# Kernel tuning notes

Hardware: AMD Instinct MI355X
Metric: run time of the kernel (lower is better)

Reference implementation:

```python
import jax, jax.numpy as jnp
import numpy as np

D = 512; H = 8; L = 6; DFF = 2048; V = 32000
B = 2; S_SRC = 1024; S_TRG = 1024
PAD_ID = 0
DH = D // H

def posenc(S, d):
    pos = np.arange(S)[:, None].astype(np.float32)
    i = np.arange(0, d, 2)[None, :].astype(np.float32)
    ang = pos / (10000.0 ** (i / d))
    pe = np.zeros((S, d), np.float32)
    pe[:, 0::2] = np.sin(ang)
    pe[:, 1::2] = np.cos(ang)
    return jnp.asarray(pe)

def layernorm(x, s, b):
    m = jnp.mean(x, -1, keepdims=True)
    v = jnp.var(x, -1, keepdims=True)
    return (x - m) * jax.lax.rsqrt(v + 1e-5) * s + b

def split_heads(x):
    b, s, _ = x.shape
    return x.reshape(b, s, H, DH).transpose(0, 2, 1, 3)  # [B,H,S,DH]

def merge_heads(x):
    b, h, s, dh = x.shape
    return x.transpose(0, 2, 1, 3).reshape(b, s, h * dh)

def attn(q, k, v, mask):
    # q,k,v: [B,H,Sq,DH]/[B,H,Sk,DH]; mask True = blocked, broadcastable to [B,H,Sq,Sk]
    scores = jnp.einsum('bhqd,bhkd->bhqk', q, k) * (DH ** -0.5)
    scores = jnp.where(mask, -1e9, scores)
    p = jax.nn.softmax(scores, axis=-1)
    return merge_heads(jnp.einsum('bhqk,bhkd->bhqd', p, v))

def setup_inputs() -> dict:
    key = jax.random.key(0)
    ks = iter(jax.random.split(key, 64))
    g = lambda shape, s=0.02: (jax.random.normal(next(ks), shape, jnp.float32) * s)
    inp = {}
    inp['batch_src'] = jax.random.randint(next(ks), (B, S_SRC), 0, V, jnp.int32)
    inp['trg_teacher'] = jax.random.randint(next(ks), (B, S_TRG), 0, V, jnp.int32)
    inp['src_emb'] = g((V, D)); inp['trg_emb'] = g((V, D))
    inp['fc_w'] = g((D, V)); inp['fc_b'] = jnp.zeros((V,), jnp.float32)
    # encoder layer stacks [L, ...]
    inp['enc_wqkv'] = g((L, D, 3 * D)); inp['enc_wo'] = g((L, D, D))
    inp['enc_ln1s'] = jnp.ones((L, D)); inp['enc_ln1b'] = jnp.zeros((L, D))
    inp['enc_w1'] = g((L, D, DFF)); inp['enc_b1'] = jnp.zeros((L, DFF))
    inp['enc_w2'] = g((L, DFF, D)); inp['enc_b2'] = jnp.zeros((L, D))
    inp['enc_ln2s'] = jnp.ones((L, D)); inp['enc_ln2b'] = jnp.zeros((L, D))
    # decoder layer stacks
    inp['dec_wqkv'] = g((L, D, 3 * D)); inp['dec_wo'] = g((L, D, D))
    inp['dec_ln1s'] = jnp.ones((L, D)); inp['dec_ln1b'] = jnp.zeros((L, D))
    inp['dec_wq'] = g((L, D, D)); inp['dec_wkv'] = g((L, D, 2 * D))
    inp['dec_woc'] = g((L, D, D))
    inp['dec_ln2s'] = jnp.ones((L, D)); inp['dec_ln2b'] = jnp.zeros((L, D))
    inp['dec_w1'] = g((L, D, DFF)); inp['dec_b1'] = jnp.zeros((L, DFF))
    inp['dec_w2'] = g((L, DFF, D)); inp['dec_b2'] = jnp.zeros((L, D))
    inp['dec_ln3s'] = jnp.ones((L, D)); inp['dec_ln3b'] = jnp.zeros((L, D))
    return inp

def reference(batch_src, trg_teacher, src_emb, trg_emb, fc_w, fc_b,
              enc_wqkv, enc_wo, enc_ln1s, enc_ln1b, enc_w1, enc_b1, enc_w2, enc_b2, enc_ln2s, enc_ln2b,
              dec_wqkv, dec_wo, dec_ln1s, dec_ln1b, dec_wq, dec_wkv, dec_woc, dec_ln2s, dec_ln2b,
              dec_w1, dec_b1, dec_w2, dec_b2, dec_ln3s, dec_ln3b):
    enc_mask = (batch_src == PAD_ID)[:, None, None, :]             # [B,1,1,S_src]
    causal = jnp.triu(jnp.ones((S_TRG, S_TRG), bool), 1)[None, None]  # [1,1,S,S]

    # ---- encoder ----
    x = src_emb[batch_src] * (D ** 0.5) + posenc(S_SRC, D)

    def enc_layer(x, p):
        wqkv, wo, l1s, l1b, w1, b1, w2, b2, l2s, l2b = p
        q, k, v = jnp.split(x @ wqkv, 3, axis=-1)
        o = attn(split_heads(q), split_heads(k), split_heads(v), enc_mask) @ wo
        x = layernorm(x + o, l1s, l1b)
        h = jax.nn.relu(x @ w1 + b1) @ w2 + b2
        return layernorm(x + h, l2s, l2b), None

    enc_out, _ = jax.lax.scan(enc_layer, x,
        (enc_wqkv, enc_wo, enc_ln1s, enc_ln1b, enc_w1, enc_b1, enc_w2, enc_b2, enc_ln2s, enc_ln2b))

    # ---- decoder (teacher forcing) ----
    y = trg_emb[trg_teacher] * (D ** 0.5) + posenc(S_TRG, D)

    def dec_layer(y, p):
        (wqkv, wo, l1s, l1b, wq, wkv, woc, l2s, l2b, w1, b1, w2, b2, l3s, l3b) = p
        q, k, v = jnp.split(y @ wqkv, 3, axis=-1)
        o = attn(split_heads(q), split_heads(k), split_heads(v), causal) @ wo
        y = layernorm(y + o, l1s, l1b)
        qc = y @ wq
        kc, vc = jnp.split(enc_out @ wkv, 2, axis=-1)
        oc = attn(split_heads(qc), split_heads(kc), split_heads(vc), enc_mask) @ woc
        y = layernorm(y + oc, l2s, l2b)
        h = jax.nn.relu(y @ w1 + b1) @ w2 + b2
        return layernorm(y + h, l3s, l3b), None

    dec_out, _ = jax.lax.scan(dec_layer, y,
        (dec_wqkv, dec_wo, dec_ln1s, dec_ln1b, dec_wq, dec_wkv, dec_woc, dec_ln2s, dec_ln2b,
         dec_w1, dec_b1, dec_w2, dec_b2, dec_ln3s, dec_ln3b))

    logits = dec_out @ fc_w + fc_b  # [B, S_TRG, V]
    return logits
```

## Files before the change

### kernel.cpp

```cpp
#include <hip/hip_runtime.h>
#include <cmath>

#define Dm   512
#define Hn   8
#define Ln   6
#define DFFm 2048
#define Vm   32000
#define Bn   2
#define Sn   1024
#define DHm  64
#define Mrows (Bn*Sn)

typedef unsigned short ushort_t;
typedef __attribute__((ext_vector_type(8))) short          s16x8;
typedef __attribute__((ext_vector_type(8))) unsigned short u16x8;
typedef __attribute__((ext_vector_type(4))) float          f32x4;

__device__ __forceinline__ ushort_t f2bf(float x) {
    union { float f; unsigned u; } un; un.f = x;
    unsigned r = un.u + 0x7fffu + ((un.u >> 16) & 1u);
    return (ushort_t)(r >> 16);
}

template<int TR, int NW>
__device__ __forceinline__ void stage_tile(const ushort_t* __restrict__ src, int ld,
                                           ushort_t* lds, int k0, int w, int lane)
{
    constexpr int CH = TR / (8 * NW);
    #pragma unroll
    for (int c = 0; c < CH; ++c) {
        const int rb = (w * CH + c) * 8;
        const int r  = rb + (lane >> 3);
        const ushort_t* gp = src + (size_t)r * ld + k0
                           + (((lane & 7) ^ ((lane >> 3) & 7)) << 3);
        __builtin_amdgcn_global_load_lds(
            (const __attribute__((address_space(1))) void*)gp,
            (__attribute__((address_space(3))) void*)(lds + rb * 64),
            16, 0, 0);
    }
}

__device__ __forceinline__ s16x8 ldrd(const ushort_t* lds, int r, int st)
{
    return *(const s16x8*)&lds[r * 64 + ((st ^ (r & 7)) << 3)];
}

template<int TM, int TN, int NW, bool OBF, bool BIAS, bool RELU, bool VTOUT, bool SWZ, bool RES>
__global__ __launch_bounds__(NW * 64) void gemm_bf(
    const ushort_t* __restrict__ A, const ushort_t* __restrict__ Bt,
    void* __restrict__ Cv, const float* __restrict__ bias,
    int K, int lda, int ldb, int ldc,
    long A_sb, long A_sh, long B_sb, long B_sh, long C_sb, long C_sh, int nh,
    ushort_t* __restrict__ VTp, int voff, long VT_sz, const float* __restrict__ Xres)
{
    constexpr int WC = NW / 2;
    constexpr int FI = TM / 32;
    constexpr int FJ = TN / (16 * WC);
    __shared__ __align__(16) ushort_t As[2][TM * 64];
    __shared__ __align__(16) ushort_t Bs[2][TN * 64];

    const int z = blockIdx.z, b = z / nh, h = z - b * nh;
    A  += (size_t)b * A_sb + (size_t)h * A_sh;
    Bt += (size_t)b * B_sb + (size_t)h * B_sh;
    ushort_t* VTl = VTp + (size_t)z * VT_sz;

    int bx = blockIdx.x, by = blockIdx.y;
    if constexpr (SWZ) {
        const int ncol = gridDim.x, nrow = gridDim.y;
        const int total = ncol * nrow;
        const int flat = bx + by * ncol;
        const int per = total >> 3;
        const int g = (flat & 7) * per + (flat >> 3);
        bx = g / nrow;
        by = g - bx * nrow;
    }

    const int tid  = threadIdx.x;
    const int w    = tid >> 6, lane = tid & 63;
    const int m0   = by * TM, n0 = bx * TN;
    const int rw   = (w / WC) * (TM / 2);
    const int cn   = (w % WC) * (TN / WC);
    const int l15  = lane & 15, l4 = lane >> 4;

    const ushort_t* Ab = A + (size_t)m0 * lda;
    const ushort_t* Bb = Bt + (size_t)n0 * ldb;

    f32x4 acc[FI][FJ] = {};

    stage_tile<TM, NW>(Ab, lda, As[0], 0, w, lane);
    stage_tile<TN, NW>(Bb, ldb, Bs[0], 0, w, lane);
    __syncthreads();

    const int nk = K >> 6;
    for (int t = 0; t < nk; ++t) {
        const int cur = t & 1;
        if (t + 1 < nk) {
            stage_tile<TM, NW>(Ab, lda, As[cur ^ 1], (t + 1) << 6, w, lane);
            stage_tile<TN, NW>(Bb, ldb, Bs[cur ^ 1], (t + 1) << 6, w, lane);
        }
        #pragma unroll
        for (int ks = 0; ks < 2; ++ks) {
            const int st = ks * 4 + l4;
            s16x8 av[FI], bv[FJ];
            #pragma unroll
            for (int i = 0; i < FI; ++i) av[i] = ldrd(As[cur], rw + i * 16 + l15, st);
            #pragma unroll
            for (int j = 0; j < FJ; ++j) bv[j] = ldrd(Bs[cur], cn + j * 16 + l15, st);
            #pragma unroll
            for (int i = 0; i < FI; ++i)
                #pragma unroll
                for (int j = 0; j < FJ; ++j)
                    acc[i][j] = __builtin_amdgcn_mfma_f32_16x16x32_bf16(
                                    av[i], bv[j], acc[i][j], 0, 0, 0);
        }
        __syncthreads();
    }

    const int colb = n0 + cn + l15;
    const int rowb = m0 + rw + (l4 << 2);
    float bvv[FJ];
    #pragma unroll
    for (int j = 0; j < FJ; ++j) bvv[j] = BIAS ? bias[colb + j * 16] : 0.f;

    if constexpr (OBF) {
        ushort_t* C = (ushort_t*)Cv + (size_t)b * C_sb + (size_t)h * C_sh;
        #pragma unroll
        for (int i = 0; i < FI; ++i)
            #pragma unroll
            for (int r = 0; r < 4; ++r) {
                const int row = rowb + i * 16 + r;
                #pragma unroll
                for (int j = 0; j < FJ; ++j) {
                    float v = acc[i][j][r] + bvv[j];
                    if (RELU) v = fmaxf(v, 0.f);
                    const int col = colb + j * 16;
                    if (VTOUT && col >= voff && col < voff + 512) {
                        const int hc = (col - voff) >> 6, d = (col - voff) & 63;
                        const int zz = (row >> 10) * 8 + hc;
                        VTl[(size_t)zz * (64 * Sn) + (size_t)d * Sn + (row & (Sn - 1))] = f2bf(v);
                    } else {
                        C[(size_t)row * ldc + col] = f2bf(v);
                    }
                }
            }
    } else {
        float* C = (float*)Cv + (size_t)b * C_sb + (size_t)h * C_sh;
        #pragma unroll
        for (int i = 0; i < FI; ++i)
            #pragma unroll
            for (int r = 0; r < 4; ++r) {
                const size_t row = rowb + i * 16 + r;
                #pragma unroll
                for (int j = 0; j < FJ; ++j) {
                    float v = acc[i][j][r] + bvv[j];
                    if (RES) v += Xres[row * ldc + colb + j * 16];
                    if (RELU) v = fmaxf(v, 0.f);
                    C[row * ldc + colb + j * 16] = v;
                }
            }
    }
}

template<int MODE>
__global__ __launch_bounds__(512) void flash_attn(
    const ushort_t* __restrict__ Qp, const ushort_t* __restrict__ Kp,
    const ushort_t* __restrict__ VTp, ushort_t* __restrict__ AO,
    const int* __restrict__ tok, int ldq, int ldk)
{
    __shared__ __align__(16) ushort_t Ks[2][2][64 * 64];
    __shared__ __align__(16) ushort_t Vs[2][2][64 * 64];
    __shared__ __align__(16) ushort_t Ps[8][16 * 64];
    __shared__ float msk[Sn];
    __shared__ float mrg[4][64][25];

    const int z = blockIdx.y, b = z >> 3, h = z & 7;
    const int qb = blockIdx.x * 64;
    const int tid = threadIdx.x, w = tid >> 6, lane = tid & 63;
    const int g = w >> 2, w4 = w & 3;
    const int l15 = lane & 15, l4 = lane >> 4;

    const ushort_t* Qbase = Qp + (size_t)b * Sn * ldq + h * 64;
    const ushort_t* Kbase = Kp + (size_t)b * Sn * ldk + h * 64;
    const ushort_t* Vbase = VTp + (size_t)z * 64 * Sn;
    ushort_t* Obase = AO + ((size_t)(b * Sn + qb)) * Dm + h * 64;

    if (MODE == 0) {
        const int* tb = tok + (size_t)b * Sn;
        for (int i = tid; i < Sn; i += 512) msk[i] = (tb[i] == 0) ? 1.f : 0.f;
    }

    const int qrow = qb + w4 * 16 + l15;
    s16x8 qv[2];
    qv[0] = *(const s16x8*)(Qbase + (size_t)qrow * ldq + l4 * 8);
    qv[1] = *(const s16x8*)(Qbase + (size_t)qrow * ldq + 32 + l4 * 8);

    f32x4 o[4] = {};
    float m[4], lsum[4];
    #pragma unroll
    for (int r = 0; r < 4; ++r) { m[r] = -1e30f; lsum[r] = 0.f; }

    const int nt = (MODE == 1) ? (qb / 64 + 1) : (Sn / 64);
    const int nIt = (nt + 1) >> 1;

    if (g < nt) {
        stage_tile<64, 4>(Kbase + (size_t)(g * 64) * ldk, ldk, Ks[g][0], 0, w4, lane);
        stage_tile<64, 4>(Vbase, Sn, Vs[g][0], g * 64, w4, lane);
    }
    __syncthreads();

    for (int it = 0; it < nIt; ++it) {
        const int kt = 2 * it + g;
        const int cur = it & 1;
        if (kt + 2 < nt) {
            stage_tile<64, 4>(Kbase + (size_t)((kt + 2) * 64) * ldk, ldk, Ks[g][cur ^ 1], 0, w4, lane);
            stage_tile<64, 4>(Vbase, Sn, Vs[g][cur ^ 1], (kt + 2) * 64, w4, lane);
        }
        if (kt < nt) {
            f32x4 s[4] = {};
            #pragma unroll
            for (int ks = 0; ks < 2; ++ks) {
                const int st = ks * 4 + l4;
                #pragma unroll
                for (int j = 0; j < 4; ++j) {
                    s16x8 bv = ldrd(Ks[g][cur], j * 16 + l15, st);
                    s[j] = __builtin_amdgcn_mfma_f32_16x16x32_bf16(qv[ks], bv, s[j], 0, 0, 0);
                }
            }

            #pragma unroll
            for (int j = 0; j < 4; ++j) {
                const int col = kt * 64 + j * 16 + l15;
                #pragma unroll
                for (int r = 0; r < 4; ++r) {
                    float v = s[j][r] * 0.125f;
                    if (MODE == 0) { if (msk[col] != 0.f) v = -1e9f; }
                    else           { if (col > qb + w4 * 16 + l4 * 4 + r) v = -1e9f; }
                    s[j][r] = v;
                }
            }

            float mt[4];
            #pragma unroll
            for (int r = 0; r < 4; ++r)
                mt[r] = fmaxf(fmaxf(s[0][r], s[1][r]), fmaxf(s[2][r], s[3][r]));
            #pragma unroll
            for (int mk = 1; mk < 16; mk <<= 1)
                #pragma unroll
                for (int r = 0; r < 4; ++r)
                    mt[r] = fmaxf(mt[r], __shfl_xor(mt[r], mk));

            float al[4];
            #pragma unroll
            for (int r = 0; r < 4; ++r) {
                const float mn = fmaxf(m[r], mt[r]);
                al[r] = __expf(m[r] - mn);
                m[r] = mn;
            }

            float rs[4] = {0.f, 0.f, 0.f, 0.f};
            ushort_t* pw = Ps[w];
            #pragma unroll
            for (int j = 0; j < 4; ++j) {
                const int slot = j * 2 + (l15 >> 3), e = l15 & 7;
                #pragma unroll
                for (int r = 0; r < 4; ++r) {
                    const float pvv = __expf(s[j][r] - m[r]);
                    rs[r] += pvv;
                    const int row = l4 * 4 + r;
                    pw[row * 64 + ((slot ^ (row & 7)) << 3) + e] = f2bf(pvv);
                }
            }
            #pragma unroll
            for (int mk = 1; mk < 16; mk <<= 1)
                #pragma unroll
                for (int r = 0; r < 4; ++r)
                    rs[r] += __shfl_xor(rs[r], mk);
            #pragma unroll
            for (int r = 0; r < 4; ++r) lsum[r] = lsum[r] * al[r] + rs[r];

            #pragma unroll
            for (int jd = 0; jd < 4; ++jd)
                #pragma unroll
                for (int r = 0; r < 4; ++r)
                    o[jd][r] *= al[r];
            #pragma unroll
            for (int ks2 = 0; ks2 < 2; ++ks2) {
                const int st2 = ks2 * 4 + l4;
                s16x8 pa = ldrd(pw, l15, st2);
                #pragma unroll
                for (int jd = 0; jd < 4; ++jd) {
                    s16x8 bv2 = ldrd(Vs[g][cur], jd * 16 + l15, st2);
                    o[jd] = __builtin_amdgcn_mfma_f32_16x16x32_bf16(pa, bv2, o[jd], 0, 0, 0);
                }
            }
        }
        __syncthreads();
    }

    if (g == 1) {
        float* mp = mrg[w4][lane];
        #pragma unroll
        for (int jd = 0; jd < 4; ++jd)
            #pragma unroll
            for (int r = 0; r < 4; ++r)
                mp[jd * 4 + r] = o[jd][r];
        #pragma unroll
        for (int r = 0; r < 4; ++r) { mp[16 + r] = m[r]; mp[20 + r] = lsum[r]; }
    }
    __syncthreads();
    if (g == 0) {
        const float* mp = mrg[w4][lane];
        float a0[4], a1[4], inv[4];
        #pragma unroll
        for (int r = 0; r < 4; ++r) {
            const float m1 = mp[16 + r];
            const float mm = fmaxf(m[r], m1);
            a0[r] = __expf(m[r] - mm);
            a1[r] = __expf(m1 - mm);
            inv[r] = 1.f / (lsum[r] * a0[r] + mp[20 + r] * a1[r]);
        }
        #pragma unroll
        for (int jd = 0; jd < 4; ++jd)
            #pragma unroll
            for (int r = 0; r < 4; ++r)
                Obase[(size_t)(w4 * 16 + l4 * 4 + r) * Dm + jd * 16 + l15] =
                    f2bf((o[jd][r] * a0[r] + mp[jd * 4 + r] * a1[r]) * inv[r]);
    }
}

struct WEnt { const float* src; ushort_t* dst; int R, C, tile0; long dls; };
struct WPack { WEnt e[12]; };

__global__ __launch_bounds__(256) void wcvt_all(WPack p)
{
    const int bid = blockIdx.x;
    int i = 0;
    #pragma unroll
    for (int k = 1; k < 12; ++k) if (bid >= p.e[k].tile0) i = k;
    const WEnt wd = p.e[i];
    const int rel = bid - wd.tile0;
    const int tC = wd.C >> 5, tR = wd.R >> 5;
    const int tpl = tC * tR;
    const int l = rel / tpl, t2 = rel - l * tpl;
    const int ty = t2 / tC, tx = t2 - ty * tC;

    const float* in  = wd.src + (size_t)l * wd.R * wd.C;
    ushort_t*    out = wd.dst + (size_t)l * wd.dls;

    __shared__ float tbuf[32][33];
    const int r0 = ty * 32, c0 = tx * 32;
    const int tid = threadIdx.x;
    const int r = tid >> 5, c = tid & 31;
    #pragma unroll
    for (int q = 0; q < 4; ++q)
        tbuf[r + q * 8][c] = in[(size_t)(r0 + r + q * 8) * wd.C + c0 + c];
    __syncthreads();
    const int c2 = tid >> 5, r2 = tid & 31;
    #pragma unroll
    for (int q = 0; q < 4; ++q)
        out[(size_t)(c0 + c2 + q * 8) * wd.R + r0 + r2] = f2bf(tbuf[r2][c2 + q * 8]);
}

__global__ __launch_bounds__(256) void ln_only(
    const float* __restrict__ s_in, float* __restrict__ x,
    const float* __restrict__ s, const float* __restrict__ bb,
    ushort_t* __restrict__ xbf)
{
    const long row = blockIdx.x;
    const int t = threadIdx.x;
    const float* sr = s_in + row * Dm;
    float v0 = sr[t];
    float v1 = sr[t + 256];

    float sum = v0 + v1, ssq = v0 * v0 + v1 * v1;
    __shared__ float red[8];
    for (int off = 32; off; off >>= 1) {
        sum += __shfl_down(sum, off);
        ssq += __shfl_down(ssq, off);
    }
    const int lane = t & 63, w = t >> 6;
    if (lane == 0) { red[w] = sum; red[4 + w] = ssq; }
    __syncthreads();
    sum = red[0] + red[1] + red[2] + red[3];
    ssq = red[4] + red[5] + red[6] + red[7];

    const float mean = sum * (1.f / Dm);
    const float var  = ssq * (1.f / Dm) - mean * mean;
    const float r = rsqrtf(var + 1e-5f);
    const float r0 = (v0 - mean) * r * s[t] + bb[t];
    const float r1 = (v1 - mean) * r * s[t + 256] + bb[t + 256];
    x[row * Dm + t] = r0; x[row * Dm + t + 256] = r1;
    xbf[row * Dm + t] = f2bf(r0);
    xbf[row * Dm + t + 256] = f2bf(r1);
}

__global__ __launch_bounds__(256) void embed_pe(
    const int* __restrict__ tokA, const float* __restrict__ embA,
    float* __restrict__ outA, ushort_t* __restrict__ outbfA,
    const int* __restrict__ tokB, const float* __restrict__ embB,
    float* __restrict__ outB, ushort_t* __restrict__ outbfB)
{
    const int bs = blockIdx.x;
    const int s = bs % Sn;
    const int t = threadIdx.x;
    const int*      tok   = blockIdx.y ? tokB : tokA;
    const float*    emb   = blockIdx.y ? embB : embA;
    float*          out   = blockIdx.y ? outB : outA;
    ushort_t*       outbf = blockIdx.y ? outbfB : outbfA;
    const int token = tok[bs];
    #pragma unroll
    for (int r = 0; r < 2; ++r) {
        const int d = t + r * 256;
        const int i = d & ~1;
        const float ang = (float)s * powf(10000.0f, -(float)i / (float)Dm);
        const float pe = (d & 1) ? cosf(ang) : sinf(ang);
        const float v = emb[(size_t)token * Dm + d] * 22.627416997969522f + pe;
        out[(size_t)bs * Dm + d] = v;
        outbf[(size_t)bs * Dm + d] = f2bf(v);
    }
}

extern "C" void kernel_launch(void* const* d_in, const int* in_sizes, int n_in,
                              void* d_out, int out_size, void* d_ws, size_t ws_size,
                              hipStream_t stream)
{
    const int*   batch_src = (const int*)d_in[0];
    const int*   trg       = (const int*)d_in[1];
    const float* src_emb   = (const float*)d_in[2];
    const float* trg_emb   = (const float*)d_in[3];
    const float* fc_w      = (const float*)d_in[4];
    const float* fc_b      = (const float*)d_in[5];
    const float* enc_wqkv  = (const float*)d_in[6];
    const float* enc_wo    = (const float*)d_in[7];
    const float* enc_ln1s  = (const float*)d_in[8];
    const float* enc_ln1b  = (const float*)d_in[9];
    const float* enc_w1    = (const float*)d_in[10];
    const float* enc_b1    = (const float*)d_in[11];
    const float* enc_w2    = (const float*)d_in[12];
    const float* enc_b2    = (const float*)d_in[13];
    const float* enc_ln2s  = (const float*)d_in[14];
    const float* enc_ln2b  = (const float*)d_in[15];
    const float* dec_wqkv  = (const float*)d_in[16];
    const float* dec_wo    = (const float*)d_in[17];
    const float* dec_ln1s  = (const float*)d_in[18];
    const float* dec_ln1b  = (const float*)d_in[19];
    const float* dec_wq    = (const float*)d_in[20];
    const float* dec_wkv   = (const float*)d_in[21];
    const float* dec_woc   = (const float*)d_in[22];
    const float* dec_ln2s  = (const float*)d_in[23];
    const float* dec_ln2b  = (const float*)d_in[24];
    const float* dec_w1    = (const float*)d_in[25];
    const float* dec_b1    = (const float*)d_in[26];
    const float* dec_w2    = (const float*)d_in[27];
    const float* dec_b2    = (const float*)d_in[28];
    const float* dec_ln3s  = (const float*)d_in[29];
    const float* dec_ln3b  = (const float*)d_in[30];
    (void)in_sizes; (void)n_in; (void)out_size; (void)ws_size;

    char* p = (char*)d_ws;
    auto alloc = [&](size_t bytes) { char* r = p; p += (bytes + 255) & ~(size_t)255; return r; };
    float*    X     = (float*)alloc((size_t)Mrows * Dm * 4);
    float*    Y     = (float*)alloc((size_t)Mrows * Dm * 4);
    float*    O     = (float*)alloc((size_t)Mrows * Dm * 4);
    ushort_t* Xbf   = (ushort_t*)alloc((size_t)Mrows * Dm * 2);
    ushort_t* Ybf   = (ushort_t*)alloc((size_t)Mrows * Dm * 2);
    ushort_t* QKVbf = (ushort_t*)alloc((size_t)Mrows * 3 * Dm * 2);
    ushort_t* QCbf  = (ushort_t*)alloc((size_t)Mrows * Dm * 2);
    ushort_t* AObf  = (ushort_t*)alloc((size_t)Mrows * Dm * 2);
    ushort_t* FHbf  = (ushort_t*)alloc((size_t)Mrows * DFFm * 2);
    ushort_t* VT    = (ushort_t*)alloc((size_t)16 * DHm * Sn * 2);
    ushort_t* KVC   = (ushort_t*)alloc((size_t)Ln * Mrows * 2 * Dm * 2);
    ushort_t* VTC   = (ushort_t*)alloc((size_t)Ln * 16 * DHm * Sn * 2);
    ushort_t* ewqkv_t = (ushort_t*)alloc((size_t)Ln * 3 * Dm * Dm * 2);
    ushort_t* ewo_t   = (ushort_t*)alloc((size_t)Ln * Dm * Dm * 2);
    ushort_t* ew1_t   = (ushort_t*)alloc((size_t)Ln * DFFm * Dm * 2);
    ushort_t* ew2_t   = (ushort_t*)alloc((size_t)Ln * Dm * DFFm * 2);
    ushort_t* dwqkv_t = (ushort_t*)alloc((size_t)Ln * 3 * Dm * Dm * 2);
    ushort_t* dwq_t   = (ushort_t*)alloc((size_t)Ln * Dm * Dm * 2);
    ushort_t* dwo_t   = (ushort_t*)alloc((size_t)Ln * Dm * Dm * 2);
    ushort_t* dwkv_t  = (ushort_t*)alloc((size_t)Ln * 2 * Dm * Dm * 2);
    ushort_t* dwoc_t  = (ushort_t*)alloc((size_t)Ln * Dm * Dm * 2);
    ushort_t* dw1_t   = (ushort_t*)alloc((size_t)Ln * DFFm * Dm * 2);
    ushort_t* dw2_t   = (ushort_t*)alloc((size_t)Ln * Dm * DFFm * 2);
    ushort_t* fcw_t   = (ushort_t*)alloc((size_t)Vm * Dm * 2);

    {
        WPack pk;
        auto set = [&](int i, const float* s, ushort_t* d, int R, int C, int nl,
                       long dls, int& acc) {
            pk.e[i] = { s, d, R, C, acc, dls };
            acc += (R >> 5) * (C >> 5) * nl;
        };
        int acc = 0;
        set(0,  enc_wqkv, ewqkv_t, Dm,   3 * Dm, Ln, (long)3 * Dm * Dm, acc);
        set(1,  enc_wo,   ewo_t,   Dm,   Dm,     Ln, (long)Dm * Dm,     acc);
        set(2,  enc_w1,   ew1_t,   Dm,   DFFm,   Ln, (long)Dm * DFFm,   acc);
        set(3,  enc_w2,   ew2_t,   DFFm, Dm,     Ln, (long)Dm * DFFm,   acc);
        set(4,  dec_wqkv, dwqkv_t, Dm,   3 * Dm, Ln, (long)3 * Dm * Dm, acc);
        set(5,  dec_wq,   dwq_t,   Dm,   Dm,     Ln, (long)Dm * Dm,     acc);
        set(6,  dec_wo,   dwo_t,   Dm,   Dm,     Ln, (long)Dm * Dm,     acc);
        set(7,  dec_wkv,  dwkv_t,  Dm,   2 * Dm, Ln, (long)2 * Dm * Dm, acc);
        set(8,  dec_woc,  dwoc_t,  Dm,   Dm,     Ln, (long)Dm * Dm,     acc);
        set(9,  dec_w1,   dw1_t,   Dm,   DFFm,   Ln, (long)Dm * DFFm,   acc);
        set(10, dec_w2,   dw2_t,   DFFm, Dm,     Ln, (long)Dm * DFFm,   acc);
        set(11, fc_w,     fcw_t,   Dm,   Vm,     1,  (long)Dm * Vm,     acc);
        wcvt_all<<<acc, 256, 0, stream>>>(pk);
    }

    embed_pe<<<dim3(Mrows, 2), 256, 0, stream>>>(
        batch_src, src_emb, X, Xbf, trg, trg_emb, Y, Ybf);

    const long VTs = (long)16 * DHm * Sn;

    for (int l = 0; l < Ln; ++l) {
        gemm_bf<64,128,4,true,false,false,true,false,false><<<dim3(12, 32, 1), 256, 0, stream>>>(
            Xbf, ewqkv_t + (size_t)l * 3 * Dm * Dm, QKVbf, nullptr,
            Dm, Dm, Dm, 3 * Dm, 0,0,0,0,0,0, 1, VT, 2 * Dm, 0, nullptr);
        flash_attn<0><<<dim3(16, 16), 512, 0, stream>>>(
            QKVbf, QKVbf + Dm, VT, AObf, batch_src, 3 * Dm, 3 * Dm);
        gemm_bf<64,64,8,false,false,false,false,false,true><<<dim3(8, 32, 1), 512, 0, stream>>>(
            AObf, ewo_t + (size_t)l * Dm * Dm, O, nullptr,
            Dm, Dm, Dm, Dm, 0,0,0,0,0,0, 1, nullptr, 0, 0, X);
        ln_only<<<Mrows, 256, 0, stream>>>(O, X, enc_ln1s + l * Dm, enc_ln1b + l * Dm, Xbf);
        gemm_bf<64,128,4,true,true,true,false,false,false><<<dim3(16, 32, 1), 256, 0, stream>>>(
            Xbf, ew1_t + (size_t)l * DFFm * Dm, FHbf, enc_b1 + l * DFFm,
            Dm, Dm, Dm, DFFm, 0,0,0,0,0,0, 1, nullptr, 0, 0, nullptr);
        gemm_bf<64,64,8,false,true,false,false,false,true><<<dim3(8, 32, 1), 512, 0, stream>>>(
            FHbf, ew2_t + (size_t)l * Dm * DFFm, O, enc_b2 + l * Dm,
            DFFm, DFFm, DFFm, Dm, 0,0,0,0,0,0, 1, nullptr, 0, 0, X);
        ln_only<<<Mrows, 256, 0, stream>>>(O, X, enc_ln2s + l * Dm, enc_ln2b + l * Dm, Xbf);
    }

    gemm_bf<64,128,4,true,false,false,true,false,false><<<dim3(8, 32, Ln), 256, 0, stream>>>(
        Xbf, dwkv_t, KVC, nullptr,
        Dm, Dm, Dm, 2 * Dm,
        0, 0, (long)2 * Dm * Dm, 0, (long)Mrows * 2 * Dm, 0, 1,
        VTC, Dm, VTs, nullptr);

    for (int l = 0; l < Ln; ++l) {
        gemm_bf<64,128,4,true,false,false,true,false,false><<<dim3(12, 32, 1), 256, 0, stream>>>(
            Ybf, dwqkv_t + (size_t)l * 3 * Dm * Dm, QKVbf, nullptr,
            Dm, Dm, Dm, 3 * Dm, 0,0,0,0,0,0, 1, VT, 2 * Dm, 0, nullptr);
        flash_attn<1><<<dim3(16, 16), 512, 0, stream>>>(
            QKVbf, QKVbf + Dm, VT, AObf, nullptr, 3 * Dm, 3 * Dm);
        gemm_bf<64,64,8,false,false,false,false,false,true><<<dim3(8, 32, 1), 512, 0, stream>>>(
            AObf, dwo_t + (size_t)l * Dm * Dm, O, nullptr,
            Dm, Dm, Dm, Dm, 0,0,0,0,0,0, 1, nullptr, 0, 0, Y);
        ln_only<<<Mrows, 256, 0, stream>>>(O, Y, dec_ln1s + l * Dm, dec_ln1b + l * Dm, Ybf);

        gemm_bf<64,64,8,true,false,false,false,false,false><<<dim3(8, 32, 1), 512, 0, stream>>>(
            Ybf, dwq_t + (size_t)l * Dm * Dm, QCbf, nullptr,
            Dm, Dm, Dm, Dm, 0,0,0,0,0,0, 1, nullptr, 0, 0, nullptr);
        flash_attn<0><<<dim3(16, 16), 512, 0, stream>>>(
            QCbf, KVC + (size_t)l * Mrows * 2 * Dm,
            VTC + (size_t)l * VTs, AObf, batch_src, Dm, 2 * Dm);
        gemm_bf<64,64,8,false,false,false,false,false,true><<<dim3(8, 32, 1), 512, 0, stream>>>(
            AObf, dwoc_t + (size_t)l * Dm * Dm, O, nullptr,
            Dm, Dm, Dm, Dm, 0,0,0,0,0,0, 1, nullptr, 0, 0, Y);
        ln_only<<<Mrows, 256, 0, stream>>>(O, Y, dec_ln2s + l * Dm, dec_ln2b + l * Dm, Ybf);

        gemm_bf<64,128,4,true,true,true,false,false,false><<<dim3(16, 32, 1), 256, 0, stream>>>(
            Ybf, dw1_t + (size_t)l * DFFm * Dm, FHbf, dec_b1 + l * DFFm,
            Dm, Dm, Dm, DFFm, 0,0,0,0,0,0, 1, nullptr, 0, 0, nullptr);
        gemm_bf<64,64,8,false,true,false,false,false,true><<<dim3(8, 32, 1), 512, 0, stream>>>(
            FHbf, dw2_t + (size_t)l * Dm * DFFm, O, dec_b2 + l * Dm,
            DFFm, DFFm, DFFm, Dm, 0,0,0,0,0,0, 1, nullptr, 0, 0, Y);
        ln_only<<<Mrows, 256, 0, stream>>>(O, Y, dec_ln3s + l * Dm, dec_ln3b + l * Dm, Ybf);
    }

    gemm_bf<128,128,4,false,true,false,false,true,false><<<dim3(Vm / 128, 16, 1), 256, 0, stream>>>(
        Ybf, fcw_t, (float*)d_out, fc_b,
        Dm, Dm, Dm, Vm, 0,0,0,0,0,0, 1, nullptr, 0, 0, nullptr);
}
```

Baseline: 1.610 ms.

## Split-K the N=512 projection GEMMs into two partials summed in layernorm

```diff
diff --git a/kernel.cpp b/kernel.cpp
--- a/kernel.cpp
+++ b/kernel.cpp
@@ -45,13 +45,13 @@
     return *(const s16x8*)&lds[r * 64 + ((st ^ (r & 7)) << 3)];
 }
 
-template<int TM, int TN, int NW, bool OBF, bool BIAS, bool RELU, bool VTOUT, bool SWZ, bool RES>
+template<int TM, int TN, int NW, bool OBF, bool BIAS, bool RELU, bool VTOUT, bool SWZ>
 __global__ __launch_bounds__(NW * 64) void gemm_bf(
     const ushort_t* __restrict__ A, const ushort_t* __restrict__ Bt,
     void* __restrict__ Cv, const float* __restrict__ bias,
     int K, int lda, int ldb, int ldc,
     long A_sb, long A_sh, long B_sb, long B_sh, long C_sb, long C_sh, int nh,
-    ushort_t* __restrict__ VTp, int voff, long VT_sz, const float* __restrict__ Xres)
+    ushort_t* __restrict__ VTp, int voff, long VT_sz)
 {
     constexpr int WC = NW / 2;
     constexpr int FI = TM / 32;
@@ -118,9 +118,10 @@
 
     const int colb = n0 + cn + l15;
     const int rowb = m0 + rw + (l4 << 2);
+    const bool doBias = BIAS && (blockIdx.z == 0);
     float bvv[FJ];
     #pragma unroll
-    for (int j = 0; j < FJ; ++j) bvv[j] = BIAS ? bias[colb + j * 16] : 0.f;
+    for (int j = 0; j < FJ; ++j) bvv[j] = doBias ? bias[colb + j * 16] : 0.f;
 
     if constexpr (OBF) {
         ushort_t* C = (ushort_t*)Cv + (size_t)b * C_sb + (size_t)h * C_sh;
@@ -153,7 +154,6 @@
                 #pragma unroll
                 for (int j = 0; j < FJ; ++j) {
                     float v = acc[i][j][r] + bvv[j];
-                    if (RES) v += Xres[row * ldc + colb + j * 16];
                     if (RELU) v = fmaxf(v, 0.f);
                     C[row * ldc + colb + j * 16] = v;
                 }
@@ -361,16 +361,17 @@
         out[(size_t)(c0 + c2 + q * 8) * wd.R + r0 + r2] = f2bf(tbuf[r2][c2 + q * 8]);
 }
 
-__global__ __launch_bounds__(256) void ln_only(
-    const float* __restrict__ s_in, float* __restrict__ x,
-    const float* __restrict__ s, const float* __restrict__ bb,
+__global__ __launch_bounds__(256) void ln_sum3(
+    const float* __restrict__ s0, const float* __restrict__ s1,
+    const float* __restrict__ xres, float* __restrict__ x,
+    const float* __restrict__ gam, const float* __restrict__ bet,
     ushort_t* __restrict__ xbf)
 {
     const long row = blockIdx.x;
     const int t = threadIdx.x;
-    const float* sr = s_in + row * Dm;
-    float v0 = sr[t];
-    float v1 = sr[t + 256];
+    const long base = row * Dm;
+    float v0 = s0[base + t]       + s1[base + t]       + xres[base + t];
+    float v1 = s0[base + t + 256] + s1[base + t + 256] + xres[base + t + 256];
 
     float sum = v0 + v1, ssq = v0 * v0 + v1 * v1;
     __shared__ float red[8];
@@ -387,11 +388,11 @@
     const float mean = sum * (1.f / Dm);
     const float var  = ssq * (1.f / Dm) - mean * mean;
     const float r = rsqrtf(var + 1e-5f);
-    const float r0 = (v0 - mean) * r * s[t] + bb[t];
-    const float r1 = (v1 - mean) * r * s[t + 256] + bb[t + 256];
-    x[row * Dm + t] = r0; x[row * Dm + t + 256] = r1;
-    xbf[row * Dm + t] = f2bf(r0);
-    xbf[row * Dm + t + 256] = f2bf(r1);
+    const float r0 = (v0 - mean) * r * gam[t] + bet[t];
+    const float r1 = (v1 - mean) * r * gam[t + 256] + bet[t + 256];
+    x[base + t] = r0; x[base + t + 256] = r1;
+    xbf[base + t] = f2bf(r0);
+    xbf[base + t + 256] = f2bf(r1);
 }
 
 __global__ __launch_bounds__(256) void embed_pe(
@@ -461,7 +462,8 @@
     auto alloc = [&](size_t bytes) { char* r = p; p += (bytes + 255) & ~(size_t)255; return r; };
     float*    X     = (float*)alloc((size_t)Mrows * Dm * 4);
     float*    Y     = (float*)alloc((size_t)Mrows * Dm * 4);
-    float*    O     = (float*)alloc((size_t)Mrows * Dm * 4);
+    float*    O     = (float*)alloc((size_t)2 * Mrows * Dm * 4);
+    float*    O1    = O + (size_t)Mrows * Dm;
     ushort_t* Xbf   = (ushort_t*)alloc((size_t)Mrows * Dm * 2);
     ushort_t* Ybf   = (ushort_t*)alloc((size_t)Mrows * Dm * 2);
     ushort_t* QKVbf = (ushort_t*)alloc((size_t)Mrows * 3 * Dm * 2);
@@ -510,65 +512,71 @@
     embed_pe<<<dim3(Mrows, 2), 256, 0, stream>>>(
         batch_src, src_emb, X, Xbf, trg, trg_emb, Y, Ybf);
 
-    const long VTs = (long)16 * DHm * Sn;
+    const long VTs  = (long)16 * DHm * Sn;
+    const long Osb  = (long)Mrows * Dm;
 
     for (int l = 0; l < Ln; ++l) {
-        gemm_bf<64,128,4,true,false,false,true,false,false><<<dim3(12, 32, 1), 256, 0, stream>>>(
+        gemm_bf<64,128,4,true,false,false,true,false><<<dim3(12, 32, 1), 256, 0, stream>>>(
             Xbf, ewqkv_t + (size_t)l * 3 * Dm * Dm, QKVbf, nullptr,
-            Dm, Dm, Dm, 3 * Dm, 0,0,0,0,0,0, 1, VT, 2 * Dm, 0, nullptr);
+            Dm, Dm, Dm, 3 * Dm, 0,0,0,0,0,0, 1, VT, 2 * Dm, 0);
         flash_attn<0><<<dim3(16, 16), 512, 0, stream>>>(
             QKVbf, QKVbf + Dm, VT, AObf, batch_src, 3 * Dm, 3 * Dm);
-        gemm_bf<64,64,8,false,false,false,false,false,true><<<dim3(8, 32, 1), 512, 0, stream>>>(
+        gemm_bf<64,64,8,false,false,false,false,false><<<dim3(8, 32, 2), 512, 0, stream>>>(
             AObf, ewo_t + (size_t)l * Dm * Dm, O, nullptr,
-            Dm, Dm, Dm, Dm, 0,0,0,0,0,0, 1, nullptr, 0, 0, X);
-        ln_only<<<Mrows, 256, 0, stream>>>(O, X, enc_ln1s + l * Dm, enc_ln1b + l * Dm, Xbf);
-        gemm_bf<64,128,4,true,true,true,false,false,false><<<dim3(16, 32, 1), 256, 0, stream>>>(
+            256, Dm, Dm, Dm, 256, 0, 256, 0, Osb, 0, 1, nullptr, 0, 0);
+        ln_sum3<<<Mrows, 256, 0, stream>>>(O, O1, X, X,
+            enc_ln1s + l * Dm, enc_ln1b + l * Dm, Xbf);
+        gemm_bf<64,128,4,true,true,true,false,false><<<dim3(16, 32, 1), 256, 0, stream>>>(
             Xbf, ew1_t + (size_t)l * DFFm * Dm, FHbf, enc_b1 + l * DFFm,
-            Dm, Dm, Dm, DFFm, 0,0,0,0,0,0, 1, nullptr, 0, 0, nullptr);
-        gemm_bf<64,64,8,false,true,false,false,false,true><<<dim3(8, 32, 1), 512, 0, stream>>>(
+            Dm, Dm, Dm, DFFm, 0,0,0,0,0,0, 1, nullptr, 0, 0);
+        gemm_bf<64,64,8,false,true,false,false,false><<<dim3(8, 32, 2), 512, 0, stream>>>(
             FHbf, ew2_t + (size_t)l * Dm * DFFm, O, enc_b2 + l * Dm,
-            DFFm, DFFm, DFFm, Dm, 0,0,0,0,0,0, 1, nullptr, 0, 0, X);
-        ln_only<<<Mrows, 256, 0, stream>>>(O, X, enc_ln2s + l * Dm, enc_ln2b + l * Dm, Xbf);
-    }
-
-    gemm_bf<64,128,4,true,false,false,true,false,false><<<dim3(8, 32, Ln), 256, 0, stream>>>(
+            1024, DFFm, DFFm, Dm, 1024, 0, 1024, 0, Osb, 0, 1, nullptr, 0, 0);
+        ln_sum3<<<Mrows, 256, 0, stream>>>(O, O1, X, X,
+            enc_ln2s + l * Dm, enc_ln2b + l * Dm, Xbf);
+    }
+
+    gemm_bf<64,128,4,true,false,false,true,false><<<dim3(8, 32, Ln), 256, 0, stream>>>(
         Xbf, dwkv_t, KVC, nullptr,
         Dm, Dm, Dm, 2 * Dm,
         0, 0, (long)2 * Dm * Dm, 0, (long)Mrows * 2 * Dm, 0, 1,
-        VTC, Dm, VTs, nullptr);
+        VTC, Dm, VTs);
 
     for (int l = 0; l < Ln; ++l) {
-        gemm_bf<64,128,4,true,false,false,true,false,false><<<dim3(12, 32, 1), 256, 0, stream>>>(
+        gemm_bf<64,128,4,true,false,false,true,false><<<dim3(12, 32, 1), 256, 0, stream>>>(
             Ybf, dwqkv_t + (size_t)l * 3 * Dm * Dm, QKVbf, nullptr,
-            Dm, Dm, Dm, 3 * Dm, 0,0,0,0,0,0, 1, VT, 2 * Dm, 0, nullptr);
+            Dm, Dm, Dm, 3 * Dm, 0,0,0,0,0,0, 1, VT, 2 * Dm, 0);
         flash_attn<1><<<dim3(16, 16), 512, 0, stream>>>(
             QKVbf, QKVbf + Dm, VT, AObf, nullptr, 3 * Dm, 3 * Dm);
-        gemm_bf<64,64,8,false,false,false,false,false,true><<<dim3(8, 32, 1), 512, 0, stream>>>(
+        gemm_bf<64,64,8,false,false,false,false,false><<<dim3(8, 32, 2), 512, 0, stream>>>(
             AObf, dwo_t + (size_t)l * Dm * Dm, O, nullptr,
-            Dm, Dm, Dm, Dm, 0,0,0,0,0,0, 1, nullptr, 0, 0, Y);
-        ln_only<<<Mrows, 256, 0, stream>>>(O, Y, dec_ln1s + l * Dm, dec_ln1b + l * Dm, Ybf);
-
-        gemm_bf<64,64,8,true,false,false,false,false,false><<<dim3(8, 32, 1), 512, 0, stream>>>(
+            256, Dm, Dm, Dm, 256, 0, 256, 0, Osb, 0, 1, nullptr, 0, 0);
+        ln_sum3<<<Mrows, 256, 0, stream>>>(O, O1, Y, Y,
+            dec_ln1s + l * Dm, dec_ln1b + l * Dm, Ybf);
+
+        gemm_bf<64,64,8,true,false,false,false,false><<<dim3(8, 32, 1), 512, 0, stream>>>(
             Ybf, dwq_t + (size_t)l * Dm * Dm, QCbf, nullptr,
-            Dm, Dm, Dm, Dm, 0,0,0,0,0,0, 1, nullptr, 0, 0, nullptr);
+            Dm, Dm, Dm, Dm, 0,0,0,0,0,0, 1, nullptr, 0, 0);
         flash_attn<0><<<dim3(16, 16), 512, 0, stream>>>(
             QCbf, KVC + (size_t)l * Mrows * 2 * Dm,
             VTC + (size_t)l * VTs, AObf, batch_src, Dm, 2 * Dm);
-        gemm_bf<64,64,8,false,false,false,false,false,true><<<dim3(8, 32, 1), 512, 0, stream>>>(
+        gemm_bf<64,64,8,false,false,false,false,false><<<dim3(8, 32, 2), 512, 0, stream>>>(
             AObf, dwoc_t + (size_t)l * Dm * Dm, O, nullptr,
-            Dm, Dm, Dm, Dm, 0,0,0,0,0,0, 1, nullptr, 0, 0, Y);
-        ln_only<<<Mrows, 256, 0, stream>>>(O, Y, dec_ln2s + l * Dm, dec_ln2b + l * Dm, Ybf);
-
-        gemm_bf<64,128,4,true,true,true,false,false,false><<<dim3(16, 32, 1), 256, 0, stream>>>(
+            256, Dm, Dm, Dm, 256, 0, 256, 0, Osb, 0, 1, nullptr, 0, 0);
+        ln_sum3<<<Mrows, 256, 0, stream>>>(O, O1, Y, Y,
+            dec_ln2s + l * Dm, dec_ln2b + l * Dm, Ybf);
+
+        gemm_bf<64,128,4,true,true,true,false,false><<<dim3(16, 32, 1), 256, 0, stream>>>(
             Ybf, dw1_t + (size_t)l * DFFm * Dm, FHbf, dec_b1 + l * DFFm,
-            Dm, Dm, Dm, DFFm, 0,0,0,0,0,0, 1, nullptr, 0, 0, nullptr);
-        gemm_bf<64,64,8,false,true,false,false,false,true><<<dim3(8, 32, 1), 512, 0, stream>>>(
+            Dm, Dm, Dm, DFFm, 0,0,0,0,0,0, 1, nullptr, 0, 0);
+        gemm_bf<64,64,8,false,true,false,false,false><<<dim3(8, 32, 2), 512, 0, stream>>>(
             FHbf, dw2_t + (size_t)l * Dm * DFFm, O, dec_b2 + l * Dm,
-            DFFm, DFFm, DFFm, Dm, 0,0,0,0,0,0, 1, nullptr, 0, 0, Y);
-        ln_only<<<Mrows, 256, 0, stream>>>(O, Y, dec_ln3s + l * Dm, dec_ln3b + l * Dm, Ybf);
-    }
-
-    gemm_bf<128,128,4,false,true,false,false,true,false><<<dim3(Vm / 128, 16, 1), 256, 0, stream>>>(
+            1024, DFFm, DFFm, Dm, 1024, 0, 1024, 0, Osb, 0, 1, nullptr, 0, 0);
+        ln_sum3<<<Mrows, 256, 0, stream>>>(O, O1, Y, Y,
+            dec_ln3s + l * Dm, dec_ln3b + l * Dm, Ybf);
+    }
+
+    gemm_bf<128,128,4,false,true,false,false,true><<<dim3(Vm / 128, 16, 1), 256, 0, stream>>>(
         Ybf, fcw_t, (float*)d_out, fc_b,
-        Dm, Dm, Dm, Vm, 0,0,0,0,0,0, 1, nullptr, 0, 0, nullptr);
-}
+        Dm, Dm, Dm, Vm, 0,0,0,0,0,0, 1, nullptr, 0, 0);
+}
```

Result: faster. 1.480 ms (-8.1%).
